# Kernel tuning notes

Hardware: AMD Instinct MI355X
Metric: run time of the kernel (lower is better)

## Reference

```python
import jax, jax.numpy as jnp
import numpy as np

N, E, F_IN, EDGE_DIM = 50000, 1600000, 128, 16
H, C = 4, 32            # heads, per-head channels for conv1/conv2
C_OUT = 2               # conv3: heads=1, out_channels=2
HC = H * C              # 128 = hidden_channels * heads
NEG_SLOPE = 0.2
BN_EPS = 1e-5


def setup_inputs() -> dict:
    key = jax.random.key(0)
    ks = jax.random.split(key, 40)
    rn = lambda k, s, sc: jax.random.normal(k, s, jnp.float32) * sc
    inp = {}
    inp["x"] = rn(ks[0], (N, F_IN), 1.0)
    inp["edge_index"] = jax.random.randint(ks[1], (2, E), 0, N, dtype=jnp.int32)
    inp["edge_attr"] = rn(ks[2], (E, EDGE_DIM), 1.0)
    # GATConv layer 1 (in=F_IN -> H x C)
    inp["W1"] = rn(ks[3], (F_IN, HC), F_IN ** -0.5)
    inp["as1"] = rn(ks[4], (H, C), 0.1)
    inp["ad1"] = rn(ks[5], (H, C), 0.1)
    inp["We1"] = rn(ks[6], (EDGE_DIM, HC), EDGE_DIM ** -0.5)
    inp["ae1"] = rn(ks[7], (H, C), 0.1)
    inp["b1"] = jnp.zeros((HC,), jnp.float32)
    # BN1 (eval mode: running stats)
    inp["g1"] = jnp.ones((HC,), jnp.float32)
    inp["be1"] = jnp.zeros((HC,), jnp.float32)
    inp["rm1"] = rn(ks[8], (HC,), 0.1)
    inp["rv1"] = jnp.ones((HC,), jnp.float32)
    # GATConv layer 2 (in=HC -> H x C)
    inp["W2"] = rn(ks[9], (HC, HC), HC ** -0.5)
    inp["as2"] = rn(ks[10], (H, C), 0.1)
    inp["ad2"] = rn(ks[11], (H, C), 0.1)
    inp["We2"] = rn(ks[12], (EDGE_DIM, HC), EDGE_DIM ** -0.5)
    inp["ae2"] = rn(ks[13], (H, C), 0.1)
    inp["b2"] = jnp.zeros((HC,), jnp.float32)
    inp["g2"] = jnp.ones((HC,), jnp.float32)
    inp["be2"] = jnp.zeros((HC,), jnp.float32)
    inp["rm2"] = rn(ks[14], (HC,), 0.1)
    inp["rv2"] = jnp.ones((HC,), jnp.float32)
    inp["W3"] = rn(ks[15], (HC, C_OUT), HC ** -0.5)
    inp["as3"] = rn(ks[16], (1, C_OUT), 0.1)
    inp["ad3"] = rn(ks[17], (1, C_OUT), 0.1)
    inp["We3"] = rn(ks[18], (EDGE_DIM, C_OUT), EDGE_DIM ** -0.5)
    inp["ae3"] = rn(ks[19], (1, C_OUT), 0.1)
    inp["b3"] = jnp.zeros((C_OUT,), jnp.float32)
    return inp


def _gat_layer(x, src, dst, eattr, W, a_s, a_d, We, a_e, b, heads, ch):
    """PyG GATConv (shared src/dst linear, edge_dim, add_self_loops already applied)."""
    n = x.shape[0]
    xp = (x @ W).reshape(n, heads, ch)                      # [N,H,C]
    alpha_src = (xp * a_s).sum(-1)                          # [N,H]
    alpha_dst = (xp * a_d).sum(-1)                          # [N,H]
    ep = (eattr @ We).reshape(-1, heads, ch)                # [E,H,C]
    alpha_e = (ep * a_e).sum(-1)                            # [E,H]
    alpha = alpha_src[src] + alpha_dst[dst] + alpha_e       # [E,H]
    alpha = jax.nn.leaky_relu(alpha, NEG_SLOPE)
    # segment softmax over incoming edges of each dst node
    m = jax.ops.segment_max(alpha, dst, num_segments=n)     # every node has a self loop
    ex = jnp.exp(alpha - m[dst])
    s = jax.ops.segment_sum(ex, dst, num_segments=n)
    alpha = ex / (s[dst] + 1e-16)                           # [E,H]
    msg = xp[src] * alpha[..., None]                        # [E,H,C]
    out = jax.ops.segment_sum(msg, dst, num_segments=n)     # [N,H,C]
    return out.reshape(n, heads * ch) + b


def _bn_eval(x, g, b, rm, rv):
    return (x - rm) * (g * jax.lax.rsqrt(rv + BN_EPS)) + b


def reference(x, edge_index, edge_attr,
              W1, as1, ad1, We1, ae1, b1, g1, be1, rm1, rv1,
              W2, as2, ad2, We2, ae2, b2, g2, be2, rm2, rv2,
              W3, as3, ad3, We3, ae3, b3):
    n = x.shape[0]
    loop = jnp.arange(n, dtype=edge_index.dtype)
    src = jnp.concatenate([edge_index[0], loop])
    dst = jnp.concatenate([edge_index[1], loop])
    # self-loop edge_attr fill_value='mean' (PyG default)
    ea_mean = jnp.broadcast_to(edge_attr.mean(0), (n, edge_attr.shape[1]))
    ea = jnp.concatenate([edge_attr, ea_mean], axis=0)

    h = _gat_layer(x, src, dst, ea, W1, as1, ad1, We1, ae1, b1, H, C)
    h = jax.nn.elu(_bn_eval(h, g1, be1, rm1, rv1))
    h = _gat_layer(h, src, dst, ea, W2, as2, ad2, We2, ae2, b2, H, C)
    h = jax.nn.elu(_bn_eval(h, g2, be2, rm2, rv2))
    out = _gat_layer(h, src, dst, ea, W3, as3, ad3, We3, ae3, b3, 1, C_OUT)
    return out
```

## Files before the change

kernel.cpp:

```cpp
#include <hip/hip_runtime.h>
#include <hip/hip_fp16.h>
#include <math.h>

#define NN 50000
#define EE 1600000
#define ETOT (EE + NN)
#define NEG_SLOPE 0.2f
#define BN_EPS 1e-5f
#define PAY_BLOCKS 1024
#define NPB 64
#define NBUCK ((NN + NPB - 1) / NPB)
#define CHUNK 8192
#define NCHUNK ((EE + CHUNK - 1) / CHUNK)


static __device__ inline unsigned pkh2(float a, float b) {
  __half ha = __float2half_rn(a), hb = __float2half_rn(b);
  unsigned short ua = *(unsigned short*)&ha, ub = *(unsigned short*)&hb;
  return ((unsigned)ub << 16) | ua;
}
static __device__ inline float upkh(unsigned u, int hi) {
  unsigned short s = hi ? (unsigned short)(u >> 16) : (unsigned short)(u & 0xffff);
  __half h = *(__half*)&s;
  return __half2float(h);
}

__global__ void compute_M_k(const float* __restrict__ We1, const float* __restrict__ ae1,
                            const float* __restrict__ We2, const float* __restrict__ ae2,
                            const float* __restrict__ We3, const float* __restrict__ ae3,
                            float* __restrict__ M) {
  int t = threadIdx.x;
  if (t < 64) {
    int d = t >> 2, h = t & 3;
    float s1 = 0.f, s2 = 0.f;
    for (int c = 0; c < 32; ++c) {
      s1 += We1[d * 128 + h * 32 + c] * ae1[h * 32 + c];
      s2 += We2[d * 128 + h * 32 + c] * ae2[h * 32 + c];
    }
    M[t] = s1;
    M[64 + t] = s2;
  }
  if (t < 16) {
    M[128 + t] = We3[t * 2] * ae3[0] + We3[t * 2 + 1] * ae3[1];
  }
}

__global__ __launch_bounds__(256) void bcount_k(const int* __restrict__ dst,
                                                const float* __restrict__ ea,
                                                int* __restrict__ bucketCnt,
                                                float* __restrict__ mean_part) {
  __shared__ int hist[1024];
  int t = threadIdx.x;
  for (int b = t; b < 1024; b += 256) hist[b] = 0;
  __syncthreads();
  float macc[16];
#pragma unroll
  for (int d = 0; d < 16; ++d) macc[d] = 0.f;
  for (int e = blockIdx.x * 256 + t; e < EE; e += PAY_BLOCKS * 256) {
    const float4* p = (const float4*)(ea + (size_t)e * 16);
    float4 q0 = p[0], q1 = p[1], q2 = p[2], q3 = p[3];
    macc[0] += q0.x; macc[1] += q0.y; macc[2] += q0.z; macc[3] += q0.w;
    macc[4] += q1.x; macc[5] += q1.y; macc[6] += q1.z; macc[7] += q1.w;
    macc[8] += q2.x; macc[9] += q2.y; macc[10] += q2.z; macc[11] += q2.w;
    macc[12] += q3.x; macc[13] += q3.y; macc[14] += q3.z; macc[15] += q3.w;
    atomicAdd(&hist[dst[e] >> 6], 1);
  }
#pragma unroll
  for (int d = 0; d < 16; ++d) {
#pragma unroll
    for (int off = 32; off; off >>= 1) macc[d] += __shfl_xor(macc[d], off, 64);
  }
  __shared__ float swsum[4][16];
  int w = t >> 6, l = t & 63;
  if (l == 0) {
#pragma unroll
    for (int d = 0; d < 16; ++d) swsum[w][d] = macc[d];
  }
  __syncthreads();
  if (t < 16) {
    mean_part[(size_t)blockIdx.x * 16 + t] =
        swsum[0][t] + swsum[1][t] + swsum[2][t] + swsum[3][t];
  }
  for (int b = t; b < NBUCK; b += 256)
    if (hist[b]) atomicAdd(&bucketCnt[b], hist[b]);
}

__global__ __launch_bounds__(256) void selfloop_k(const float* __restrict__ mean_part,
                                                  const float* __restrict__ M,
                                                  float* __restrict__ alpha_sl) {
  __shared__ float s[256];
  int t = threadIdx.x;
  int d = t & 15, c = t >> 4;
  float v = 0.f;
  for (int i = c * 64; i < (c + 1) * 64; ++i) v += mean_part[(size_t)i * 16 + d];
  s[t] = v;
  __syncthreads();
  if (t < 16) {
    float sum = 0.f;
    for (int c2 = 0; c2 < 16; ++c2) sum += s[c2 * 16 + t];
    s[t] = sum / (float)EE;
  }
  __syncthreads();
  if (t < 9) {
    float r = 0.f;
    if (t < 4) {
      for (int dd = 0; dd < 16; ++dd) r += s[dd] * M[dd * 4 + t];
    } else if (t < 8) {
      int h = t - 4;
      for (int dd = 0; dd < 16; ++dd) r += s[dd] * M[64 + dd * 4 + h];
    } else {
      for (int dd = 0; dd < 16; ++dd) r += s[dd] * M[128 + dd];
    }
    alpha_sl[t] = r;
  }
}

__global__ __launch_bounds__(1024) void bscan_k(const int* __restrict__ bucketCnt,
                                                int* __restrict__ pBase,
                                                int* __restrict__ rBase,
                                                int* __restrict__ bcur) {
  __shared__ int s1[1024], s2[1024];
  int t = threadIdx.x;
  int cnt = (t < NBUCK) ? bucketCnt[t] : 0;
  int nn = 0;
  if (t < NBUCK) {
    int n0 = t * NPB;
    nn = NN - n0; if (nn > NPB) nn = NPB;
  }
  s1[t] = cnt;
  s2[t] = cnt + nn;
  __syncthreads();
  for (int off = 1; off < 1024; off <<= 1) {
    int a = (t >= off) ? s1[t - off] : 0;
    int b = (t >= off) ? s2[t - off] : 0;
    __syncthreads();
    s1[t] += a; s2[t] += b;
    __syncthreads();
  }
  if (t < NBUCK) {
    pBase[t] = s1[t] - cnt;
    rBase[t] = s2[t] - (cnt + nn);
    bcur[t] = s1[t] - cnt;
  }
  if (t == 0) { pBase[NBUCK] = EE; rBase[NBUCK] = ETOT; }
}

__global__ __launch_bounds__(256) void bscat_k(const int* __restrict__ dst,
                                               const int* __restrict__ src,
                                               int* __restrict__ bcur,
                                               uint2* __restrict__ pairs) {
  __shared__ int hist[1024];
  __shared__ int ofs[1024];
  int t = threadIdx.x;
  for (int c = blockIdx.x; c < NCHUNK; c += gridDim.x) {
    int cb = c * CHUNK;
    for (int b = t; b < 1024; b += 256) hist[b] = 0;
    __syncthreads();
#pragma unroll
    for (int k = 0; k < 8; ++k) {
      int e = cb + k * 1024 + t * 4;
      if (e < EE) {
        int4 d4 = *(const int4*)&dst[e];
        atomicAdd(&hist[d4.x >> 6], 1);
        atomicAdd(&hist[d4.y >> 6], 1);
        atomicAdd(&hist[d4.z >> 6], 1);
        atomicAdd(&hist[d4.w >> 6], 1);
      }
    }
    __syncthreads();
    for (int b = t; b < NBUCK; b += 256) {
      int h = hist[b];
      ofs[b] = h ? atomicAdd(&bcur[b], h) : 0;
      hist[b] = 0;
    }
    __syncthreads();
#pragma unroll
    for (int k = 0; k < 8; ++k) {
      int e = cb + k * 1024 + t * 4;
      if (e < EE) {
        int4 d4 = *(const int4*)&dst[e];
        int4 s4 = *(const int4*)&src[e];
        int dd[4] = {d4.x, d4.y, d4.z, d4.w};
        int sv[4] = {s4.x, s4.y, s4.z, s4.w};
#pragma unroll
        for (int j = 0; j < 4; ++j) {
          int b = dd[j] >> 6;
          int pos = ofs[b] + atomicAdd(&hist[b], 1);
          pairs[pos] = make_uint2(((unsigned)(dd[j] & (NPB - 1)) << 21) | (unsigned)(e + j),
                                  (unsigned)sv[j]);
        }
      }
    }
    __syncthreads();
  }
}

__global__ __launch_bounds__(256) void cbuild_k(const int* __restrict__ pBase,
                                                const int* __restrict__ rBase,
                                                const uint2* __restrict__ pairs,
                                                const float* __restrict__ ea,
                                                const float* __restrict__ M,
                                                const float* __restrict__ asl,
                                                uint2* __restrict__ recAE1,
                                                uint2* __restrict__ recAE2,
                                                float* __restrict__ rec3,
                                                int* __restrict__ recSrc,
                                                int* __restrict__ row_ofs) {
  __shared__ float sM[144];
  __shared__ int lcnt[NPB];
  __shared__ int ss[NPB];
  __shared__ int cur[NPB];
  __shared__ float sEA[256 * 17];
  __shared__ uint2 sPr[256];
  int b = blockIdx.x;
  int t = threadIdx.x;
  if (t < 144) sM[t] = M[t];
  if (t < NPB) lcnt[t] = 0;
  __syncthreads();
  int n0 = b * NPB;
  int n1 = n0 + NPB; if (n1 > NN) n1 = NN;
  int nn = n1 - n0;
  int pb = pBase[b], pe = pBase[b + 1];
  for (int i = pb + t; i < pe; i += 256) atomicAdd(&lcnt[pairs[i].x >> 21], 1);
  __syncthreads();
  int v = (t < nn) ? (lcnt[t] + 1) : 0;
  if (t < NPB) ss[t] = v;
  __syncthreads();
  for (int off = 1; off < NPB; off <<= 1) {
    int a = (t >= off && t < NPB) ? ss[t - off] : 0;
    __syncthreads();
    if (t < NPB) ss[t] += a;
    __syncthreads();
  }
  int rb = rBase[b];
  if (t < nn) {
    int self = rb + ss[t] - v;
    row_ofs[n0 + t] = self;
    cur[t] = self + 1;
    recAE1[self] = make_uint2(pkh2(asl[0], asl[1]), pkh2(asl[2], asl[3]));
    recAE2[self] = make_uint2(pkh2(asl[4], asl[5]), pkh2(asl[6], asl[7]));
    rec3[self] = asl[8];
    recSrc[self] = n0 + t;
  }
  if (b == NBUCK - 1 && t == 0) row_ofs[NN] = ETOT;
  __syncthreads();

  int qid = t >> 2;
  int l = t & 3;
  for (int base2 = pb; base2 < pe; base2 += 256) {
    int cnt = pe - base2; if (cnt > 256) cnt = 256;
#pragma unroll
    for (int k = 0; k < 4; ++k) {
      int r = k * 64 + qid;
      if (r < cnt) {
        uint2 u = pairs[base2 + r];
        if (l == 0) sPr[r] = u;
        float4 q = *(const float4*)(ea + (size_t)(u.x & 0x1FFFFF) * 16 + l * 4);
        int o = r * 17 + l * 4;
        sEA[o + 0] = q.x; sEA[o + 1] = q.y; sEA[o + 2] = q.z; sEA[o + 3] = q.w;
      }
    }
    __syncthreads();
    if (t < cnt) {
      uint2 u = sPr[t];
      float a1[4] = {0.f, 0.f, 0.f, 0.f}, a2[4] = {0.f, 0.f, 0.f, 0.f};
      float a3 = 0.f;
#pragma unroll
      for (int d = 0; d < 16; ++d) {
        float vv = sEA[t * 17 + d];
#pragma unroll
        for (int h = 0; h < 4; ++h) {
          a1[h] += vv * sM[d * 4 + h];
          a2[h] += vv * sM[64 + d * 4 + h];
        }
        a3 += vv * sM[128 + d];
      }
      int pos = atomicAdd(&cur[u.x >> 21], 1);
      recAE1[pos] = make_uint2(pkh2(a1[0], a1[1]), pkh2(a1[2], a1[3]));
      recAE2[pos] = make_uint2(pkh2(a2[0], a2[1]), pkh2(a2[2], a2[3]));
      rec3[pos] = a3;
      recSrc[pos] = (int)u.y;
    }
    __syncthreads();
  }
}

__global__ __launch_bounds__(256) void gemm128a_k(const float* __restrict__ X,
                                                  const float* __restrict__ W,
                                                  const float* __restrict__ as,
                                                  const float* __restrict__ ad,
                                                  __half* __restrict__ Y,
                                                  float* __restrict__ asrc,
                                                  float* __restrict__ adst,
                                                  int nrows) {
  __shared__ float sW[128 * 64];
  __shared__ float sX[64 * 132];
  __shared__ float sas[128], sad[128];
  int t = threadIdx.x;
  int r0 = blockIdx.x * 64;
  int cb = blockIdx.y;
  if (t < 128) { sas[t] = as[t]; sad[t] = ad[t]; }
#pragma unroll
  for (int i = 0; i < 8; ++i) {
    int flat = t + i * 256;
    int k = flat >> 4, c4 = flat & 15;
    *(float4*)&sW[k * 64 + c4 * 4] = *(const float4*)&W[k * 128 + cb * 64 + c4 * 4];
  }
  int rows = nrows - r0; if (rows > 64) rows = 64;
#pragma unroll
  for (int i = 0; i < 8; ++i) {
    int flat = t + i * 256;
    int r = flat >> 5, k4 = flat & 31;
    if (r < rows)
      *(float4*)&sX[r * 132 + k4 * 4] = *(const float4*)&X[(size_t)(r0 + r) * 128 + k4 * 4];
  }
  __syncthreads();
  int cq = t & 15, rl = t >> 4;
  float4 acc[4];
#pragma unroll
  for (int i = 0; i < 4; ++i) acc[i] = make_float4(0.f, 0.f, 0.f, 0.f);

  for (int k = 0; k < 128; k += 4) {
    float4 w0 = *(float4*)&sW[(k + 0) * 64 + cq * 4];
    float4 w1 = *(float4*)&sW[(k + 1) * 64 + cq * 4];
    float4 w2 = *(float4*)&sW[(k + 2) * 64 + cq * 4];
    float4 w3 = *(float4*)&sW[(k + 3) * 64 + cq * 4];
#pragma unroll
    for (int i = 0; i < 4; ++i) {
      float4 xv = *(float4*)&sX[(rl + i * 16) * 132 + k];
      acc[i].x += xv.x * w0.x + xv.y * w1.x + xv.z * w2.x + xv.w * w3.x;
      acc[i].y += xv.x * w0.y + xv.y * w1.y + xv.z * w2.y + xv.w * w3.y;
      acc[i].z += xv.x * w0.z + xv.y * w1.z + xv.z * w2.z + xv.w * w3.z;
      acc[i].w += xv.x * w0.w + xv.y * w1.w + xv.z * w2.w + xv.w * w3.w;
    }
  }
  int h = cb * 2 + (cq >> 3);
  int col0 = cb * 64 + cq * 4;
#pragma unroll
  for (int i = 0; i < 4; ++i) {
    int r = rl + i * 16;
    if (r < rows) {
      uint2 st;
      st.x = pkh2(acc[i].x, acc[i].y);
      st.y = pkh2(acc[i].z, acc[i].w);
      *(uint2*)&Y[(size_t)(r0 + r) * 128 + col0] = st;
      float s1 = acc[i].x * sas[col0] + acc[i].y * sas[col0 + 1] +
                 acc[i].z * sas[col0 + 2] + acc[i].w * sas[col0 + 3];
      float s2 = acc[i].x * sad[col0] + acc[i].y * sad[col0 + 1] +
                 acc[i].z * sad[col0 + 2] + acc[i].w * sad[col0 + 3];
      s1 += __shfl_xor(s1, 1, 8); s1 += __shfl_xor(s1, 2, 8); s1 += __shfl_xor(s1, 4, 8);
      s2 += __shfl_xor(s2, 1, 8); s2 += __shfl_xor(s2, 2, 8); s2 += __shfl_xor(s2, 4, 8);
      if ((cq & 7) == 0) {
        asrc[(size_t)(r0 + r) * 4 + h] = s1;
        adst[(size_t)(r0 + r) * 4 + h] = s2;
      }
    }
  }
}

__global__ __launch_bounds__(128) void agg128_k(
    const int* __restrict__ row_ofs, const unsigned* __restrict__ recAE,
    const int* __restrict__ recSrc, const __half* __restrict__ xp,
    const float* __restrict__ asrc, const float* __restrict__ adst,
    const float* __restrict__ bias, const float* __restrict__ g,
    const float* __restrict__ be, const float* __restrict__ rm,
    const float* __restrict__ rv, float* __restrict__ out) {
  int n = blockIdx.x;
  int t = threadIdx.x;
  int h = t >> 5, j = t & 31;
  int e4 = t >> 4, gg = t & 15;
  int hh = gg >> 2;
  __shared__ float s_w[4 * 64];
  __shared__ int s_src[64];
  __shared__ float sf[4], sden[4];
  __shared__ float sacc[8][132];
  int beg = row_ofs[n], end = row_ofs[n + 1];
  float adn = adst[(size_t)n * 4 + h];
  float m_run = -1e30f, s_run = 0.f;
  float acc[8];
#pragma unroll
  for (int i = 0; i < 8; ++i) acc[i] = 0.f;

  for (int base = beg; base < end; base += 64) {
    int cnt = end - base; if (cnt > 64) cnt = 64;
    float a0 = -1e30f, a1 = -1e30f;
    if (j < cnt) {
      int idx = base + j;
      float ae = upkh(recAE[(size_t)idx * 2 + (h >> 1)], h & 1);
      int sj = recSrc[idx];
      if (h == 0) s_src[j] = sj;
      float a = asrc[(size_t)sj * 4 + h] + adn + ae;
      a0 = (a > 0.f) ? a : NEG_SLOPE * a;
    }
    if (j + 32 < cnt) {
      int idx = base + j + 32;
      float ae = upkh(recAE[(size_t)idx * 2 + (h >> 1)], h & 1);
      int sj = recSrc[idx];
      if (h == 0) s_src[j + 32] = sj;
      float a = asrc[(size_t)sj * 4 + h] + adn + ae;
      a1 = (a > 0.f) ? a : NEG_SLOPE * a;
    }
    float cm = fmaxf(a0, a1);
#pragma unroll
    for (int off = 16; off; off >>= 1) cm = fmaxf(cm, __shfl_xor(cm, off, 32));
    float f = 1.f;
    if (cm > m_run) { f = expf(m_run - cm); s_run *= f; m_run = cm; }
    if (j == 0) sf[h] = f;
    float ex0 = (j < cnt) ? expf(a0 - m_run) : 0.f;
    float ex1 = (j + 32 < cnt) ? expf(a1 - m_run) : 0.f;
    s_w[h * 64 + j] = ex0;
    s_w[h * 64 + j + 32] = ex1;
    float se = ex0 + ex1;
#pragma unroll
    for (int off = 16; off; off >>= 1) se += __shfl_xor(se, off, 32);
    s_run += se;
    __syncthreads();
    float ff = sf[hh];
    if (ff != 1.f) {
#pragma unroll
      for (int i = 0; i < 8; ++i) acc[i] *= ff;
    }
    for (int e2 = 0; e2 < cnt; e2 += 16) {
      int ed0 = e2 + e4, ed1 = e2 + e4 + 8;
      bool b0 = ed0 < cnt, b1 = ed1 < cnt;
      uint4 v0, v1;
      float w0 = 0.f, w1 = 0.f;
      if (b0) {
        int s0 = s_src[ed0]; w0 = s_w[hh * 64 + ed0];
        v0 = *(const uint4*)&xp[(size_t)s0 * 128 + gg * 8];
      }
      if (b1) {
        int s1 = s_src[ed1]; w1 = s_w[hh * 64 + ed1];
        v1 = *(const uint4*)&xp[(size_t)s1 * 128 + gg * 8];
      }
      if (b0) {
        acc[0] += w0 * upkh(v0.x, 0); acc[1] += w0 * upkh(v0.x, 1);
        acc[2] += w0 * upkh(v0.y, 0); acc[3] += w0 * upkh(v0.y, 1);
        acc[4] += w0 * upkh(v0.z, 0); acc[5] += w0 * upkh(v0.z, 1);
        acc[6] += w0 * upkh(v0.w, 0); acc[7] += w0 * upkh(v0.w, 1);
      }
      if (b1) {
        acc[0] += w1 * upkh(v1.x, 0); acc[1] += w1 * upkh(v1.x, 1);
        acc[2] += w1 * upkh(v1.y, 0); acc[3] += w1 * upkh(v1.y, 1);
        acc[4] += w1 * upkh(v1.z, 0); acc[5] += w1 * upkh(v1.z, 1);
        acc[6] += w1 * upkh(v1.w, 0); acc[7] += w1 * upkh(v1.w, 1);
      }
    }
    __syncthreads();
  }
  if (j == 0) sden[h] = s_run;
#pragma unroll
  for (int i = 0; i < 8; ++i) sacc[e4][gg * 8 + i] = acc[i];
  __syncthreads();
  float v = 0.f;
#pragma unroll
  for (int i = 0; i < 8; ++i) v += sacc[i][t];
  v = v / (sden[t >> 5] + 1e-16f) + bias[t];
  v = (v - rm[t]) * (g[t] * rsqrtf(rv[t] + BN_EPS)) + be[t];
  v = (v > 0.f) ? v : (expf(v) - 1.f);
  out[(size_t)n * 128 + t] = v;
}

__global__ __launch_bounds__(256) void xp3_k(const float* __restrict__ h2,
                                             const float* __restrict__ W3,
                                             const float* __restrict__ as3,
                                             const float* __restrict__ ad3,
                                             float* __restrict__ xp3,
                                             float* __restrict__ asrc3,
                                             float* __restrict__ adst3) {
  __shared__ float sW[256];
  int t = threadIdx.x;
  sW[t] = W3[t];
  __syncthreads();
  int n = blockIdx.x * 256 + t;
  if (n < NN) {
    const float4* row = (const float4*)(h2 + (size_t)n * 128);
    float y0 = 0.f, y1 = 0.f;
#pragma unroll
    for (int i = 0; i < 32; ++i) {
      float4 v = row[i];
      y0 += v.x * sW[(i * 4 + 0) * 2] + v.y * sW[(i * 4 + 1) * 2] +
            v.z * sW[(i * 4 + 2) * 2] + v.w * sW[(i * 4 + 3) * 2];
      y1 += v.x * sW[(i * 4 + 0) * 2 + 1] + v.y * sW[(i * 4 + 1) * 2 + 1] +
            v.z * sW[(i * 4 + 2) * 2 + 1] + v.w * sW[(i * 4 + 3) * 2 + 1];
    }
    xp3[n * 2] = y0;
    xp3[n * 2 + 1] = y1;
    asrc3[n] = y0 * as3[0] + y1 * as3[1];
    adst3[n] = y0 * ad3[0] + y1 * ad3[1];
  }
}

__global__ __launch_bounds__(256) void agg2_k(const int* __restrict__ row_ofs,
                                              const float* __restrict__ rec3,
                                              const int* __restrict__ recSrc,
                                              const float* __restrict__ xp3,
                                              const float* __restrict__ asrc3,
                                              const float* __restrict__ adst3,
                                              const float* __restrict__ b3,
                                              float* __restrict__ out) {
  int t = threadIdx.x;
  int w = t >> 6, l = t & 63;
  int n = blockIdx.x * 4 + w;
  if (n >= NN) return;
  int beg = row_ofs[n], end = row_ofs[n + 1];
  float adn = adst3[n];
  float m = -1e30f, s = 0.f, a0 = 0.f, a1 = 0.f;
  for (int idx = beg + l; idx < end; idx += 64) {
    float aev = rec3[idx];
    int sj = recSrc[idx];
    float a = asrc3[sj] + adn + aev;
    a = (a > 0.f) ? a : NEG_SLOPE * a;
    if (a > m) {
      float f = expf(m - a);
      s *= f; a0 *= f; a1 *= f; m = a;
    }
    float ex = expf(a - m);
    s += ex;
    a0 += ex * xp3[sj * 2];
    a1 += ex * xp3[sj * 2 + 1];
  }
  float M = m;
#pragma unroll
  for (int off = 32; off; off >>= 1) M = fmaxf(M, __shfl_xor(M, off, 64));
  float f = expf(m - M);
  s *= f; a0 *= f; a1 *= f;
#pragma unroll
  for (int off = 32; off; off >>= 1) {
    s += __shfl_xor(s, off, 64);
    a0 += __shfl_xor(a0, off, 64);
    a1 += __shfl_xor(a1, off, 64);
  }
  if (l == 0) {
    float inv = 1.f / (s + 1e-16f);
    out[n * 2] = a0 * inv + b3[0];
    out[n * 2 + 1] = a1 * inv + b3[1];
  }
}

extern "C" void kernel_launch(void* const* d_in, const int* in_sizes, int n_in,
                              void* d_out, int out_size, void* d_ws, size_t ws_size,
                              hipStream_t stream) {
  const float* x   = (const float*)d_in[0];
  const int*   ei  = (const int*)d_in[1];
  const float* ea  = (const float*)d_in[2];
  const float* W1  = (const float*)d_in[3];
  const float* as1 = (const float*)d_in[4];
  const float* ad1 = (const float*)d_in[5];
  const float* We1 = (const float*)d_in[6];
  const float* ae1 = (const float*)d_in[7];
  const float* b1  = (const float*)d_in[8];
  const float* g1  = (const float*)d_in[9];
  const float* be1 = (const float*)d_in[10];
  const float* rm1 = (const float*)d_in[11];
  const float* rv1 = (const float*)d_in[12];
  const float* W2  = (const float*)d_in[13];
  const float* as2 = (const float*)d_in[14];
  const float* ad2 = (const float*)d_in[15];
  const float* We2 = (const float*)d_in[16];
  const float* ae2 = (const float*)d_in[17];
  const float* b2  = (const float*)d_in[18];
  const float* g2  = (const float*)d_in[19];
  const float* be2 = (const float*)d_in[20];
  const float* rm2 = (const float*)d_in[21];
  const float* rv2 = (const float*)d_in[22];
  const float* W3  = (const float*)d_in[23];
  const float* as3 = (const float*)d_in[24];
  const float* ad3 = (const float*)d_in[25];
  const float* We3 = (const float*)d_in[26];
  const float* ae3 = (const float*)d_in[27];
  const float* b3  = (const float*)d_in[28];

  const int* srcA = ei;
  const int* dstA = ei + EE;

  char* p = (char*)d_ws;
  auto alloc = [&](size_t bytes) -> void* {
    void* r = (void*)p;
    p += (bytes + 255) & ~(size_t)255;
    return r;
  };
  uint2* recAE1 = (uint2*)alloc(sizeof(uint2) * (size_t)ETOT);
  uint2* recAE2 = (uint2*)alloc(sizeof(uint2) * (size_t)ETOT);
  float* rec3   = (float*)alloc(sizeof(float) * (size_t)ETOT);
  int*   recSrc = (int*)alloc(sizeof(int) * (size_t)ETOT);
  uint2* pairs  = (uint2*)alloc(sizeof(uint2) * (size_t)EE);
  __half* xp    = (__half*)alloc(sizeof(__half) * (size_t)NN * 128);
  float* hbuf   = (float*)alloc(sizeof(float) * (size_t)NN * 128);
  float* Mbuf   = (float*)alloc(sizeof(float) * 144);
  float* meanp  = (float*)alloc(sizeof(float) * (size_t)PAY_BLOCKS * 16);
  float* asl    = (float*)alloc(sizeof(float) * 12);
  float* asrc   = (float*)alloc(sizeof(float) * (size_t)NN * 4);
  float* adst   = (float*)alloc(sizeof(float) * (size_t)NN * 4);
  float* xp3    = (float*)alloc(sizeof(float) * (size_t)NN * 2);
  float* asrc3  = (float*)alloc(sizeof(float) * (size_t)NN);
  float* adst3  = (float*)alloc(sizeof(float) * (size_t)NN);
  int* bucketCnt = (int*)alloc(sizeof(int) * (size_t)NBUCK);
  int* pBase    = (int*)alloc(sizeof(int) * (size_t)(NBUCK + 1));
  int* rBase    = (int*)alloc(sizeof(int) * (size_t)(NBUCK + 1));
  int* bcur     = (int*)alloc(sizeof(int) * (size_t)NBUCK);
  int* row_ofs  = (int*)alloc(sizeof(int) * (size_t)(NN + 1));

  hipMemsetAsync(bucketCnt, 0, NBUCK * sizeof(int), stream);

  compute_M_k<<<1, 64, 0, stream>>>(We1, ae1, We2, ae2, We3, ae3, Mbuf);
  bcount_k<<<PAY_BLOCKS, 256, 0, stream>>>(dstA, ea, bucketCnt, meanp);
  selfloop_k<<<1, 256, 0, stream>>>(meanp, Mbuf, asl);
  bscan_k<<<1, 1024, 0, stream>>>(bucketCnt, pBase, rBase, bcur);
  bscat_k<<<200, 256, 0, stream>>>(dstA, srcA, bcur, pairs);
  cbuild_k<<<NBUCK, 256, 0, stream>>>(pBase, rBase, pairs, ea, Mbuf, asl,
                                      recAE1, recAE2, rec3, recSrc, row_ofs);

  gemm128a_k<<<dim3((NN + 63) / 64, 2), 256, 0, stream>>>(x, W1, as1, ad1, xp, asrc, adst, NN);
  agg128_k<<<NN, 128, 0, stream>>>(row_ofs, (const unsigned*)recAE1, recSrc, xp,
                                   asrc, adst, b1, g1, be1, rm1, rv1, hbuf);
  gemm128a_k<<<dim3((NN + 63) / 64, 2), 256, 0, stream>>>(hbuf, W2, as2, ad2, xp, asrc, adst, NN);
  agg128_k<<<NN, 128, 0, stream>>>(row_ofs, (const unsigned*)recAE2, recSrc, xp,
                                   asrc, adst, b2, g2, be2, rm2, rv2, hbuf);
  xp3_k<<<(NN + 255) / 256, 256, 0, stream>>>(hbuf, W3, as3, ad3, xp3, asrc3, adst3);
  agg2_k<<<(NN + 3) / 4, 256, 0, stream>>>(row_ofs, rec3, recSrc, xp3, asrc3, adst3,
                                           b3, (float*)d_out);
}
```

Baseline: 392.2 us.

## Fuse edge-attr mean reduction into cbuild and move self-loop records to separate kernel

Removes the separate full streaming pass over edge_attr in bcount_k by accumulating the per-dimension sums inside cbuild_k, which already gathers every edge's attributes into shared memory. bcount_k now only histograms dst, using int4 loads and 256 blocks. Because the mean is now known only after cbuild, a new slrec_k kernel writes the self-loop records afterward, and selfloop_k is reordered and sums over per-bucket partials. This saves one read of the 100MB edge_attr array at the cost of an extra small kernel launch and extra register pressure in cbuild.

```diff
diff --git a/kernel.cpp b/kernel.cpp
--- a/kernel.cpp
+++ b/kernel.cpp
@@ -7,7 +7,6 @@
 #define ETOT (EE + NN)
 #define NEG_SLOPE 0.2f
 #define BN_EPS 1e-5f
-#define PAY_BLOCKS 1024
 #define NPB 64
 #define NBUCK ((NN + NPB - 1) / NPB)
 #define CHUNK 8192
@@ -46,41 +45,19 @@
 }
 
 __global__ __launch_bounds__(256) void bcount_k(const int* __restrict__ dst,
-                                                const float* __restrict__ ea,
-                                                int* __restrict__ bucketCnt,
-                                                float* __restrict__ mean_part) {
+                                                int* __restrict__ bucketCnt) {
   __shared__ int hist[1024];
   int t = threadIdx.x;
   for (int b = t; b < 1024; b += 256) hist[b] = 0;
   __syncthreads();
-  float macc[16];
-#pragma unroll
-  for (int d = 0; d < 16; ++d) macc[d] = 0.f;
-  for (int e = blockIdx.x * 256 + t; e < EE; e += PAY_BLOCKS * 256) {
-    const float4* p = (const float4*)(ea + (size_t)e * 16);
-    float4 q0 = p[0], q1 = p[1], q2 = p[2], q3 = p[3];
-    macc[0] += q0.x; macc[1] += q0.y; macc[2] += q0.z; macc[3] += q0.w;
-    macc[4] += q1.x; macc[5] += q1.y; macc[6] += q1.z; macc[7] += q1.w;
-    macc[8] += q2.x; macc[9] += q2.y; macc[10] += q2.z; macc[11] += q2.w;
-    macc[12] += q3.x; macc[13] += q3.y; macc[14] += q3.z; macc[15] += q3.w;
-    atomicAdd(&hist[dst[e] >> 6], 1);
-  }
-#pragma unroll
-  for (int d = 0; d < 16; ++d) {
-#pragma unroll
-    for (int off = 32; off; off >>= 1) macc[d] += __shfl_xor(macc[d], off, 64);
-  }
-  __shared__ float swsum[4][16];
-  int w = t >> 6, l = t & 63;
-  if (l == 0) {
-#pragma unroll
-    for (int d = 0; d < 16; ++d) swsum[w][d] = macc[d];
-  }
-  __syncthreads();
-  if (t < 16) {
-    mean_part[(size_t)blockIdx.x * 16 + t] =
-        swsum[0][t] + swsum[1][t] + swsum[2][t] + swsum[3][t];
-  }
+  for (int e = (blockIdx.x * 256 + t) * 4; e < EE; e += gridDim.x * 1024) {
+    int4 d4 = *(const int4*)&dst[e];
+    atomicAdd(&hist[d4.x >> 6], 1);
+    atomicAdd(&hist[d4.y >> 6], 1);
+    atomicAdd(&hist[d4.z >> 6], 1);
+    atomicAdd(&hist[d4.w >> 6], 1);
+  }
+  __syncthreads();
   for (int b = t; b < NBUCK; b += 256)
     if (hist[b]) atomicAdd(&bucketCnt[b], hist[b]);
 }
@@ -92,7 +69,7 @@
   int t = threadIdx.x;
   int d = t & 15, c = t >> 4;
   float v = 0.f;
-  for (int i = c * 64; i < (c + 1) * 64; ++i) v += mean_part[(size_t)i * 16 + d];
+  for (int i = c; i < NBUCK; i += 16) v += mean_part[(size_t)i * 16 + d];
   s[t] = v;
   __syncthreads();
   if (t < 16) {
@@ -115,6 +92,22 @@
   }
 }
 
+__global__ __launch_bounds__(256) void slrec_k(const int* __restrict__ row_ofs,
+                                               const float* __restrict__ asl,
+                                               uint2* __restrict__ recAE1,
+                                               uint2* __restrict__ recAE2,
+                                               float* __restrict__ rec3,
+                                               int* __restrict__ recSrc) {
+  int n = blockIdx.x * 256 + threadIdx.x;
+  if (n < NN) {
+    int p = row_ofs[n];
+    recAE1[p] = make_uint2(pkh2(asl[0], asl[1]), pkh2(asl[2], asl[3]));
+    recAE2[p] = make_uint2(pkh2(asl[4], asl[5]), pkh2(asl[6], asl[7]));
+    rec3[p] = asl[8];
+    recSrc[p] = n;
+  }
+}
+
 __global__ __launch_bounds__(1024) void bscan_k(const int* __restrict__ bucketCnt,
                                                 int* __restrict__ pBase,
                                                 int* __restrict__ rBase,
@@ -200,18 +193,19 @@
                                                 const uint2* __restrict__ pairs,
                                                 const float* __restrict__ ea,
                                                 const float* __restrict__ M,
-                                                const float* __restrict__ asl,
                                                 uint2* __restrict__ recAE1,
                                                 uint2* __restrict__ recAE2,
                                                 float* __restrict__ rec3,
                                                 int* __restrict__ recSrc,
-                                                int* __restrict__ row_ofs) {
+                                                int* __restrict__ row_ofs,
+                                                float* __restrict__ mean_part) {
   __shared__ float sM[144];
   __shared__ int lcnt[NPB];
   __shared__ int ss[NPB];
   __shared__ int cur[NPB];
   __shared__ float sEA[256 * 17];
   __shared__ uint2 sPr[256];
+  __shared__ float swsum[4][16];
   int b = blockIdx.x;
   int t = threadIdx.x;
   if (t < 144) sM[t] = M[t];
@@ -237,16 +231,15 @@
     int self = rb + ss[t] - v;
     row_ofs[n0 + t] = self;
     cur[t] = self + 1;
-    recAE1[self] = make_uint2(pkh2(asl[0], asl[1]), pkh2(asl[2], asl[3]));
-    recAE2[self] = make_uint2(pkh2(asl[4], asl[5]), pkh2(asl[6], asl[7]));
-    rec3[self] = asl[8];
-    recSrc[self] = n0 + t;
   }
   if (b == NBUCK - 1 && t == 0) row_ofs[NN] = ETOT;
   __syncthreads();
 
   int qid = t >> 2;
   int l = t & 3;
+  float macc[16];
+#pragma unroll
+  for (int d = 0; d < 16; ++d) macc[d] = 0.f;
   for (int base2 = pb; base2 < pe; base2 += 256) {
     int cnt = pe - base2; if (cnt > 256) cnt = 256;
 #pragma unroll
@@ -268,6 +261,7 @@
 #pragma unroll
       for (int d = 0; d < 16; ++d) {
         float vv = sEA[t * 17 + d];
+        macc[d] += vv;
 #pragma unroll
         for (int h = 0; h < 4; ++h) {
           a1[h] += vv * sM[d * 4 + h];
@@ -282,6 +276,21 @@
       recSrc[pos] = (int)u.y;
     }
     __syncthreads();
+  }
+#pragma unroll
+  for (int d = 0; d < 16; ++d) {
+#pragma unroll
+    for (int off = 32; off; off >>= 1) macc[d] += __shfl_xor(macc[d], off, 64);
+  }
+  int w = t >> 6, l2 = t & 63;
+  if (l2 == 0) {
+#pragma unroll
+    for (int d = 0; d < 16; ++d) swsum[w][d] = macc[d];
+  }
+  __syncthreads();
+  if (t < 16) {
+    mean_part[(size_t)b * 16 + t] =
+        swsum[0][t] + swsum[1][t] + swsum[2][t] + swsum[3][t];
   }
 }
 
@@ -588,7 +597,7 @@
   __half* xp    = (__half*)alloc(sizeof(__half) * (size_t)NN * 128);
   float* hbuf   = (float*)alloc(sizeof(float) * (size_t)NN * 128);
   float* Mbuf   = (float*)alloc(sizeof(float) * 144);
-  float* meanp  = (float*)alloc(sizeof(float) * (size_t)PAY_BLOCKS * 16);
+  float* meanp  = (float*)alloc(sizeof(float) * (size_t)NBUCK * 16);
   float* asl    = (float*)alloc(sizeof(float) * 12);
   float* asrc   = (float*)alloc(sizeof(float) * (size_t)NN * 4);
   float* adst   = (float*)alloc(sizeof(float) * (size_t)NN * 4);
@@ -604,12 +613,13 @@
   hipMemsetAsync(bucketCnt, 0, NBUCK * sizeof(int), stream);
 
   compute_M_k<<<1, 64, 0, stream>>>(We1, ae1, We2, ae2, We3, ae3, Mbuf);
-  bcount_k<<<PAY_BLOCKS, 256, 0, stream>>>(dstA, ea, bucketCnt, meanp);
-  selfloop_k<<<1, 256, 0, stream>>>(meanp, Mbuf, asl);
+  bcount_k<<<256, 256, 0, stream>>>(dstA, bucketCnt);
   bscan_k<<<1, 1024, 0, stream>>>(bucketCnt, pBase, rBase, bcur);
   bscat_k<<<200, 256, 0, stream>>>(dstA, srcA, bcur, pairs);
-  cbuild_k<<<NBUCK, 256, 0, stream>>>(pBase, rBase, pairs, ea, Mbuf, asl,
-                                      recAE1, recAE2, rec3, recSrc, row_ofs);
+  cbuild_k<<<NBUCK, 256, 0, stream>>>(pBase, rBase, pairs, ea, Mbuf,
+                                      recAE1, recAE2, rec3, recSrc, row_ofs, meanp);
+  selfloop_k<<<1, 256, 0, stream>>>(meanp, Mbuf, asl);
+  slrec_k<<<(NN + 255) / 256, 256, 0, stream>>>(row_ofs, asl, recAE1, recAE2, rec3, recSrc);
 
   gemm128a_k<<<dim3((NN + 63) / 64, 2), 256, 0, stream>>>(x, W1, as1, ad1, xp, asrc, adst, NN);
   agg128_k<<<NN, 128, 0, stream>>>(row_ofs, (const unsigned*)recAE1, recSrc, xp,
```

Result: faster. 376.8 us (-3.9%).
